# Optimization experiments

Hardware: AMD Instinct MI355X
Metric: run time of the kernel (lower is better)

The kernel has to match this reference:

```python
import jax, jax.numpy as jnp
import numpy as np

B, Q, D, N = 128, 20, 11, 100000  # batch, produced vectors per sample, feature dim, song DB size
EPS = 1e-8  # torch cosine_similarity eps


def setup_inputs() -> dict:
    key = jax.random.key(0)
    ks = jax.random.split(key, 8)
    x = jax.random.normal(ks[0], (B, 5, 11), dtype=jnp.float32)
    W1 = jax.random.normal(ks[1], (55, 128), dtype=jnp.float32) * 0.1
    b1 = jnp.zeros((128,), dtype=jnp.float32)
    W2 = jax.random.normal(ks[2], (128, 64), dtype=jnp.float32) * 0.1
    b2 = jnp.zeros((64,), dtype=jnp.float32)
    W3 = jax.random.normal(ks[3], (64, Q * D), dtype=jnp.float32) * 0.1
    b3 = jnp.zeros((Q * D,), dtype=jnp.float32)
    songs = jax.random.normal(ks[4], (N, D), dtype=jnp.float32)
    return {"x": x, "W1": W1, "b1": b1, "W2": W2, "b2": b2, "W3": W3, "b3": b3, "songs": songs}


def reference(x, W1, b1, W2, b2, W3, b3, songs):
    # Encoder MLP: Flatten -> Linear -> ReLU -> Linear -> ReLU -> Linear
    h = x.reshape(x.shape[0], -1)                 # [B, 55]
    h = jax.nn.relu(h @ W1 + b1)                  # [B, 128]
    h = jax.nn.relu(h @ W2 + b2)                  # [B, 64]
    produced = (h @ W3 + b3).reshape(-1, Q, D)    # [B, 20, 11]

    # Batched cosine-similarity kNN (k=1 / argmax) against the song DB.
    # torch cosine_similarity: a.b / (max(||a||, eps) * max(||b||, eps))
    p_norm = produced / jnp.maximum(jnp.linalg.norm(produced, axis=-1, keepdims=True), EPS)
    s_norm = songs / jnp.maximum(jnp.linalg.norm(songs, axis=-1, keepdims=True), EPS)
    sim = jnp.einsum('bqd,nd->bqn', p_norm, s_norm)  # [B, Q, N]
    best = jnp.argmax(sim, axis=-1)                  # [B, Q]
    return songs[best]                                # [B, Q, D]
```

## Files before the change

kernel.cpp:

```cpp
#include <hip/hip_runtime.h>
#include <math.h>

#define EPS 1e-8f

constexpr int B_ = 128;
constexpr int Q_ = 20;
constexpr int D_ = 11;
constexpr int N_ = 100000;
constexpr int DP_ = 12;
constexpr int NPAIR = B_ * Q_;
constexpr int NCH = 1000;
constexpr int CS = N_ / NCH;
constexpr int NG = CS / 4;
constexpr int STPB = 128;
constexpr int PPT = 4;
constexpr int REP = NPAIR / (PPT * STPB);

__global__ void prep_kernel(const float* __restrict__ x,
                            const float* __restrict__ W1, const float* __restrict__ b1,
                            const float* __restrict__ W2, const float* __restrict__ b2,
                            const float* __restrict__ W3, const float* __restrict__ b3,
                            const float* __restrict__ songs,
                            float* __restrict__ pnorm, float* __restrict__ snorm,
                            int do_snorm)
{
    const int t = threadIdx.x;
    if (blockIdx.x >= B_) {
        if (!do_snorm) return;
        const int i = (blockIdx.x - B_) * blockDim.x + t;
        if (i >= N_) return;
        float v[DP_]; float ss = 0.0f;
#pragma unroll
        for (int d = 0; d < D_; ++d) { v[d] = songs[(size_t)i * D_ + d]; ss += v[d] * v[d]; }
        float nrm = fmaxf(sqrtf(ss), EPS);
#pragma unroll
        for (int d = 0; d < D_; ++d) v[d] /= nrm;
        v[D_] = 0.0f;
        float4* o = reinterpret_cast<float4*>(snorm + (size_t)i * DP_);
        o[0] = make_float4(v[0], v[1], v[2], v[3]);
        o[1] = make_float4(v[4], v[5], v[6], v[7]);
        o[2] = make_float4(v[8], v[9], v[10], v[11]);
        return;
    }
    __shared__ float xr[55];
    __shared__ float h1[128];
    __shared__ float h2[64];
    __shared__ float prod[220];
    const int b = blockIdx.x;
    if (t < 55) xr[t] = x[b * 55 + t];
    __syncthreads();
    if (t < 128) {
        float s = b1[t];
        for (int k = 0; k < 55; ++k) s += xr[k] * W1[k * 128 + t];
        h1[t] = fmaxf(s, 0.0f);
    }
    __syncthreads();
    if (t < 64) {
        float s = b2[t];
        for (int k = 0; k < 128; ++k) s += h1[k] * W2[k * 64 + t];
        h2[t] = fmaxf(s, 0.0f);
    }
    __syncthreads();
    if (t < 220) {
        float s = b3[t];
        for (int k = 0; k < 64; ++k) s += h2[k] * W3[k * 220 + t];
        prod[t] = s;
    }
    __syncthreads();
    if (t < Q_) {
        float ss = 0.0f;
        for (int d = 0; d < D_; ++d) { float v = prod[t * D_ + d]; ss += v * v; }
        float nrm = fmaxf(sqrtf(ss), EPS);
        float* o = pnorm + (b * Q_ + t) * DP_;
        for (int d = 0; d < D_; ++d) o[d] = prod[t * D_ + d] / nrm;
        o[D_] = 0.0f;
    }
}

__device__ __forceinline__ float dot11(const float* __restrict__ q,
                                       const float4 a, const float4 b, const float4 c)
{
    float x = q[0] * a.x;
    x = fmaf(q[1], a.y, x);
    x = fmaf(q[2], a.z, x);
    x = fmaf(q[3], a.w, x);
    x = fmaf(q[4], b.x, x);
    x = fmaf(q[5], b.y, x);
    x = fmaf(q[6], b.z, x);
    x = fmaf(q[7], b.w, x);
    x = fmaf(q[8], c.x, x);
    x = fmaf(q[9], c.y, x);
    x = fmaf(q[10], c.z, x);
    return x;
}

__device__ __forceinline__ unsigned int fkey(float f)
{
    unsigned int b = __float_as_uint(f);
    return (b & 0x80000000u) ? ~b : (b | 0x80000000u);
}

__device__ __forceinline__ unsigned long long pack_vi(float v, int idx)
{
    return ((unsigned long long)fkey(v) << 32) | (unsigned long long)(0xFFFFFFFFu - (unsigned int)idx);
}

__global__ __launch_bounds__(STPB, 4)
void sim7_kernel(const float* __restrict__ pnorm,
                 const float* __restrict__ snorm,
                 unsigned long long* __restrict__ res)
{
    __shared__ __align__(16) float lds[CS * DP_];
    const int bid = blockIdx.x;
    const int u = bid & 7;
    const int k = bid >> 3;
    const int r = k % REP;
    const int m = k / REP;
    const int chunk = u + 8 * m;
    const int t = threadIdx.x;

    const float4* src = reinterpret_cast<const float4*>(snorm) + (size_t)chunk * CS * 3;
    float4* l4 = reinterpret_cast<float4*>(lds);
    for (int i = t; i < CS * 3; i += STPB) l4[i] = src[i];

    const int jb = r * (PPT * STPB) + t;
    float qv[PPT][D_];
#pragma unroll
    for (int p = 0; p < PPT; ++p) {
        const float4* q4 = reinterpret_cast<const float4*>(pnorm + (size_t)(jb + p * STPB) * DP_);
        float4 qa = q4[0], qb = q4[1], qc = q4[2];
        qv[p][0] = qa.x; qv[p][1] = qa.y; qv[p][2]  = qa.z; qv[p][3] = qa.w;
        qv[p][4] = qb.x; qv[p][5] = qb.y; qv[p][6]  = qb.z; qv[p][7] = qb.w;
        qv[p][8] = qc.x; qv[p][9] = qc.y; qv[p][10] = qc.z;
    }
    __syncthreads();

    float bv[PPT]; int gi[PPT];
#pragma unroll
    for (int p = 0; p < PPT; ++p) { bv[p] = -1e30f; gi[p] = 0; }

    const float4* vg = l4;
    for (int g = 0; g < NG; ++g, vg += 12) {
        float4 v0 = vg[0], v1 = vg[1], v2 = vg[2], v3 = vg[3], v4 = vg[4], v5 = vg[5];
        float a0[PPT], a1[PPT];
#pragma unroll
        for (int p = 0; p < PPT; ++p) {
            a0[p] = dot11(qv[p], v0, v1, v2);
            a1[p] = dot11(qv[p], v3, v4, v5);
        }
        float4 w0 = vg[6], w1 = vg[7], w2 = vg[8], w3 = vg[9], w4 = vg[10], w5 = vg[11];
#pragma unroll
        for (int p = 0; p < PPT; ++p) {
            float a2 = dot11(qv[p], w0, w1, w2);
            float a3 = dot11(qv[p], w3, w4, w5);
            float mx = fmaxf(fmaxf(a0[p], a1[p]), fmaxf(a2, a3));
            if (mx > bv[p]) { bv[p] = mx; gi[p] = g; }
        }
    }

#pragma unroll
    for (int p = 0; p < PPT; ++p) {
        const float4* wg = l4 + gi[p] * 12;
        float a0 = dot11(qv[p], wg[0], wg[1],  wg[2]);
        float a1 = dot11(qv[p], wg[3], wg[4],  wg[5]);
        float a2 = dot11(qv[p], wg[6], wg[7],  wg[8]);
        float a3 = dot11(qv[p], wg[9], wg[10], wg[11]);
        int base = chunk * CS + gi[p] * 4;
        int idx = base;
        if (a3 == bv[p]) idx = base + 3;
        if (a2 == bv[p]) idx = base + 2;
        if (a1 == bv[p]) idx = base + 1;
        if (a0 == bv[p]) idx = base;
        atomicMax(&res[jb + p * STPB], pack_vi(bv[p], idx));
    }
}

template<int FNCH>
__global__ void sim6f_kernel(const float* __restrict__ pnorm,
                             const float* __restrict__ songs,
                             unsigned long long* __restrict__ res)
{
    constexpr int FCS = N_ / FNCH;
    const int chunk = blockIdx.x;
    const int j = blockIdx.y * 256 + threadIdx.x;

    float qv[D_];
#pragma unroll
    for (int d = 0; d < D_; ++d) qv[d] = pnorm[j * DP_ + d];

    float bestv = -1e30f;
    int   besti = 0;
    const int base = chunk * FCS;
    for (int i = base; i < base + FCS; ++i) {
        float sv[D_]; float ss = 0.0f;
#pragma unroll
        for (int d = 0; d < D_; ++d) { sv[d] = songs[(size_t)i * D_ + d]; ss += sv[d] * sv[d]; }
        float nrm = fmaxf(sqrtf(ss), EPS);
        float a = qv[0] * (sv[0] / nrm);
#pragma unroll
        for (int d = 1; d < D_; ++d) a = fmaf(qv[d], sv[d] / nrm, a);
        if (a > bestv) { bestv = a; besti = i; }
    }
    atomicMax(&res[j], pack_vi(bestv, besti));
}

__global__ void gather_kernel(const unsigned long long* __restrict__ res,
                              const float* __restrict__ songs, float* __restrict__ out)
{
    const int j = blockIdx.x * blockDim.x + threadIdx.x;
    if (j >= NPAIR) return;
    const unsigned int idx = 0xFFFFFFFFu - (unsigned int)(res[j] & 0xFFFFFFFFull);
#pragma unroll
    for (int d = 0; d < D_; ++d) out[(size_t)j * D_ + d] = songs[(size_t)idx * D_ + d];
}

extern "C" void kernel_launch(void* const* d_in, const int* in_sizes, int n_in,
                              void* d_out, int out_size, void* d_ws, size_t ws_size,
                              hipStream_t stream)
{
    const float* x     = (const float*)d_in[0];
    const float* W1    = (const float*)d_in[1];
    const float* b1    = (const float*)d_in[2];
    const float* W2    = (const float*)d_in[3];
    const float* b2    = (const float*)d_in[4];
    const float* W3    = (const float*)d_in[5];
    const float* b3    = (const float*)d_in[6];
    const float* songs = (const float*)d_in[7];
    float* out = (float*)d_out;

    constexpr size_t PN = (size_t)NPAIR * DP_;
    constexpr size_t SN = (size_t)N_ * DP_;
    float* pnorm = (float*)d_ws;
    constexpr int SNB = (N_ + 255) / 256;

    const size_t need_full = (PN + SN) * sizeof(float) + (size_t)NPAIR * 8 + 64;
    const size_t need_min  = PN * sizeof(float) + (size_t)NPAIR * 8 + 64;

    if (ws_size >= need_full) {
        float* snorm = pnorm + PN;
        unsigned long long* res =
            (unsigned long long*)(((uintptr_t)(snorm + SN) + 7) & ~(uintptr_t)7);
        hipMemsetAsync(res, 0, (size_t)NPAIR * 8, stream);
        prep_kernel<<<B_ + SNB, 256, 0, stream>>>(x, W1, b1, W2, b2, W3, b3, songs,
                                                  pnorm, snorm, 1);
        sim7_kernel<<<NCH * REP, STPB, 0, stream>>>(pnorm, snorm, res);
        gather_kernel<<<(NPAIR + 255) / 256, 256, 0, stream>>>(res, songs, out);
    } else if (ws_size >= need_min) {
        unsigned long long* res =
            (unsigned long long*)(((uintptr_t)(pnorm + PN) + 7) & ~(uintptr_t)7);
        hipMemsetAsync(res, 0, (size_t)NPAIR * 8, stream);
        prep_kernel<<<B_, 256, 0, stream>>>(x, W1, b1, W2, b2, W3, b3, songs,
                                            pnorm, nullptr, 0);
        constexpr int FNCH = 250;
        sim6f_kernel<FNCH><<<dim3(FNCH, NPAIR / 256), 256, 0, stream>>>(pnorm, songs, res);
        gather_kernel<<<(NPAIR + 255) / 256, 256, 0, stream>>>(res, songs, out);
    }
}
```

Measured before the change: 92.78 us.

## Read song vectors directly from global memory with one wavefront per block

Removes the LDS staging of each song chunk and the block barrier, so each 64-thread block (one wavefront) reads the normalized song vectors straight from global memory. The addresses are uniform across the wave, so the compiler can turn them into scalar loads. Pairs per thread rise from 4 to 8 to get more reuse of each loaded song vector. This trades shared-memory traffic and sync for scalar/global loads and higher register pressure under the existing launch bounds.

```diff
diff --git a/kernel.cpp b/kernel.cpp
--- a/kernel.cpp
+++ b/kernel.cpp
@@ -12,8 +12,8 @@
 constexpr int NCH = 1000;
 constexpr int CS = N_ / NCH;
 constexpr int NG = CS / 4;
-constexpr int STPB = 128;
-constexpr int PPT = 4;
+constexpr int STPB = 64;
+constexpr int PPT = 8;
 constexpr int REP = NPAIR / (PPT * STPB);
 
 __global__ void prep_kernel(const float* __restrict__ x,
@@ -77,20 +77,20 @@
     }
 }
 
-__device__ __forceinline__ float dot11(const float* __restrict__ q,
-                                       const float4 a, const float4 b, const float4 c)
-{
-    float x = q[0] * a.x;
-    x = fmaf(q[1], a.y, x);
-    x = fmaf(q[2], a.z, x);
-    x = fmaf(q[3], a.w, x);
-    x = fmaf(q[4], b.x, x);
-    x = fmaf(q[5], b.y, x);
-    x = fmaf(q[6], b.z, x);
-    x = fmaf(q[7], b.w, x);
-    x = fmaf(q[8], c.x, x);
-    x = fmaf(q[9], c.y, x);
-    x = fmaf(q[10], c.z, x);
+__device__ __forceinline__ float dot11s(const float* __restrict__ q,
+                                        const float* __restrict__ s)
+{
+    float x = q[0] * s[0];
+    x = fmaf(q[1],  s[1],  x);
+    x = fmaf(q[2],  s[2],  x);
+    x = fmaf(q[3],  s[3],  x);
+    x = fmaf(q[4],  s[4],  x);
+    x = fmaf(q[5],  s[5],  x);
+    x = fmaf(q[6],  s[6],  x);
+    x = fmaf(q[7],  s[7],  x);
+    x = fmaf(q[8],  s[8],  x);
+    x = fmaf(q[9],  s[9],  x);
+    x = fmaf(q[10], s[10], x);
     return x;
 }
 
@@ -106,24 +106,19 @@
 }
 
 __global__ __launch_bounds__(STPB, 4)
-void sim7_kernel(const float* __restrict__ pnorm,
+void sim8_kernel(const float* __restrict__ pnorm,
                  const float* __restrict__ snorm,
                  unsigned long long* __restrict__ res)
 {
-    __shared__ __align__(16) float lds[CS * DP_];
     const int bid = blockIdx.x;
     const int u = bid & 7;
     const int k = bid >> 3;
     const int r = k % REP;
     const int m = k / REP;
     const int chunk = u + 8 * m;
-    const int t = threadIdx.x;
-
-    const float4* src = reinterpret_cast<const float4*>(snorm) + (size_t)chunk * CS * 3;
-    float4* l4 = reinterpret_cast<float4*>(lds);
-    for (int i = t; i < CS * 3; i += STPB) l4[i] = src[i];
-
-    const int jb = r * (PPT * STPB) + t;
+    const int lane = threadIdx.x;
+
+    const int jb = r * (PPT * STPB) + lane;
     float qv[PPT][D_];
 #pragma unroll
     for (int p = 0; p < PPT; ++p) {
@@ -133,38 +128,33 @@
         qv[p][4] = qb.x; qv[p][5] = qb.y; qv[p][6]  = qb.z; qv[p][7] = qb.w;
         qv[p][8] = qc.x; qv[p][9] = qc.y; qv[p][10] = qc.z;
     }
-    __syncthreads();
 
     float bv[PPT]; int gi[PPT];
 #pragma unroll
     for (int p = 0; p < PPT; ++p) { bv[p] = -1e30f; gi[p] = 0; }
 
-    const float4* vg = l4;
-    for (int g = 0; g < NG; ++g, vg += 12) {
-        float4 v0 = vg[0], v1 = vg[1], v2 = vg[2], v3 = vg[3], v4 = vg[4], v5 = vg[5];
-        float a0[PPT], a1[PPT];
+    const float* cb = snorm + (size_t)chunk * CS * DP_;
+
+    for (int g = 0; g < NG; ++g) {
+        const float* sb = cb + g * (4 * DP_);
 #pragma unroll
         for (int p = 0; p < PPT; ++p) {
-            a0[p] = dot11(qv[p], v0, v1, v2);
-            a1[p] = dot11(qv[p], v3, v4, v5);
-        }
-        float4 w0 = vg[6], w1 = vg[7], w2 = vg[8], w3 = vg[9], w4 = vg[10], w5 = vg[11];
-#pragma unroll
-        for (int p = 0; p < PPT; ++p) {
-            float a2 = dot11(qv[p], w0, w1, w2);
-            float a3 = dot11(qv[p], w3, w4, w5);
-            float mx = fmaxf(fmaxf(a0[p], a1[p]), fmaxf(a2, a3));
+            float a0 = dot11s(qv[p], sb);
+            float a1 = dot11s(qv[p], sb + DP_);
+            float a2 = dot11s(qv[p], sb + 2 * DP_);
+            float a3 = dot11s(qv[p], sb + 3 * DP_);
+            float mx = fmaxf(fmaxf(a0, a1), fmaxf(a2, a3));
             if (mx > bv[p]) { bv[p] = mx; gi[p] = g; }
         }
     }
 
 #pragma unroll
     for (int p = 0; p < PPT; ++p) {
-        const float4* wg = l4 + gi[p] * 12;
-        float a0 = dot11(qv[p], wg[0], wg[1],  wg[2]);
-        float a1 = dot11(qv[p], wg[3], wg[4],  wg[5]);
-        float a2 = dot11(qv[p], wg[6], wg[7],  wg[8]);
-        float a3 = dot11(qv[p], wg[9], wg[10], wg[11]);
+        const float* sb = cb + gi[p] * (4 * DP_);
+        float a0 = dot11s(qv[p], sb);
+        float a1 = dot11s(qv[p], sb + DP_);
+        float a2 = dot11s(qv[p], sb + 2 * DP_);
+        float a3 = dot11s(qv[p], sb + 3 * DP_);
         int base = chunk * CS + gi[p] * 4;
         int idx = base;
         if (a3 == bv[p]) idx = base + 3;
@@ -243,7 +233,7 @@
         hipMemsetAsync(res, 0, (size_t)NPAIR * 8, stream);
         prep_kernel<<<B_ + SNB, 256, 0, stream>>>(x, W1, b1, W2, b2, W3, b3, songs,
                                                   pnorm, snorm, 1);
-        sim7_kernel<<<NCH * REP, STPB, 0, stream>>>(pnorm, snorm, res);
+        sim8_kernel<<<NCH * REP, STPB, 0, stream>>>(pnorm, snorm, res);
         gather_kernel<<<(NPAIR + 255) / 256, 256, 0, stream>>>(res, songs, out);
     } else if (ws_size >= need_min) {
         unsigned long long* res =
```

New measurement: 118.8 us. +28.0%, slower.

## Give each block all query pairs over two song chunks with register prefetch

Applied to the files above, without the earlier changes.

Replaces the sim7 grid (1000 chunks × 5 query groups, 4 queries per thread) with 500 blocks of 256 threads. Each block covers all 2560 query vectors at 10 per thread and walks two song chunks in sequence. The second chunk is loaded into registers while the first chunk is processed, then written to LDS. This raises per-thread register reuse of song vectors, reduces redundant LDS loads of song data, and cuts atomics per song chunk. It costs heavy register pressure (110 query floats per thread), launch bounds of 1, and far fewer resident waves, which can hurt latency hiding.

```diff
diff --git a/kernel.cpp b/kernel.cpp
--- a/kernel.cpp
+++ b/kernel.cpp
@@ -12,9 +12,10 @@
 constexpr int NCH = 1000;
 constexpr int CS = N_ / NCH;
 constexpr int NG = CS / 4;
-constexpr int STPB = 128;
-constexpr int PPT = 4;
-constexpr int REP = NPAIR / (PPT * STPB);
+constexpr int TPB10 = 256;
+constexpr int PPT10 = 10;
+constexpr int CPB = 2;
+constexpr int NBLK = NCH / CPB;
 
 __global__ void prep_kernel(const float* __restrict__ x,
                             const float* __restrict__ W1, const float* __restrict__ b1,
@@ -105,29 +106,56 @@
     return ((unsigned long long)fkey(v) << 32) | (unsigned long long)(0xFFFFFFFFu - (unsigned int)idx);
 }
 
-__global__ __launch_bounds__(STPB, 4)
-void sim7_kernel(const float* __restrict__ pnorm,
-                 const float* __restrict__ snorm,
-                 unsigned long long* __restrict__ res)
-{
-    __shared__ __align__(16) float lds[CS * DP_];
+__device__ __forceinline__ void chunk_pass(const float4* __restrict__ l4,
+                                           const float qv[PPT10][D_],
+                                           float* __restrict__ bv, int* __restrict__ gi,
+                                           int goff)
+{
+    const float4* vg = l4;
+    for (int g = 0; g < NG; ++g, vg += 12) {
+        float4 v0 = vg[0], v1 = vg[1], v2 = vg[2], v3 = vg[3], v4 = vg[4], v5 = vg[5];
+        float a0[PPT10], a1[PPT10];
+#pragma unroll
+        for (int p = 0; p < PPT10; ++p) {
+            a0[p] = dot11(qv[p], v0, v1, v2);
+            a1[p] = dot11(qv[p], v3, v4, v5);
+        }
+        float4 w0 = vg[6], w1 = vg[7], w2 = vg[8], w3 = vg[9], w4 = vg[10], w5 = vg[11];
+#pragma unroll
+        for (int p = 0; p < PPT10; ++p) {
+            float a2 = dot11(qv[p], w0, w1, w2);
+            float a3 = dot11(qv[p], w3, w4, w5);
+            float mx = fmaxf(fmaxf(a0[p], a1[p]), fmaxf(a2, a3));
+            if (mx > bv[p]) { bv[p] = mx; gi[p] = goff + g; }
+        }
+    }
+}
+
+__global__ __launch_bounds__(TPB10, 1)
+void sim10_kernel(const float* __restrict__ pnorm,
+                  const float* __restrict__ snorm,
+                  unsigned long long* __restrict__ res)
+{
+    __shared__ __align__(16) float lds[CPB][CS * DP_];
     const int bid = blockIdx.x;
-    const int u = bid & 7;
-    const int k = bid >> 3;
-    const int r = k % REP;
-    const int m = k / REP;
-    const int chunk = u + 8 * m;
     const int t = threadIdx.x;
-
-    const float4* src = reinterpret_cast<const float4*>(snorm) + (size_t)chunk * CS * 3;
-    float4* l4 = reinterpret_cast<float4*>(lds);
-    for (int i = t; i < CS * 3; i += STPB) l4[i] = src[i];
-
-    const int jb = r * (PPT * STPB) + t;
-    float qv[PPT][D_];
-#pragma unroll
-    for (int p = 0; p < PPT; ++p) {
-        const float4* q4 = reinterpret_cast<const float4*>(pnorm + (size_t)(jb + p * STPB) * DP_);
+    const int c0 = bid * CPB;
+
+    const float4* s40 = reinterpret_cast<const float4*>(snorm) + (size_t)c0 * CS * 3;
+    const float4* s41 = s40 + CS * 3;
+    float4* b0 = reinterpret_cast<float4*>(lds[0]);
+    float4* b1 = reinterpret_cast<float4*>(lds[1]);
+
+    b0[t] = s40[t];
+    if (t < CS * 3 - TPB10) b0[t + TPB10] = s40[t + TPB10];
+    float4 r0 = s41[t];
+    float4 r1 = make_float4(0.f, 0.f, 0.f, 0.f);
+    if (t < CS * 3 - TPB10) r1 = s41[t + TPB10];
+
+    float qv[PPT10][D_];
+#pragma unroll
+    for (int p = 0; p < PPT10; ++p) {
+        const float4* q4 = reinterpret_cast<const float4*>(pnorm + (size_t)(t + p * TPB10) * DP_);
         float4 qa = q4[0], qb = q4[1], qc = q4[2];
         qv[p][0] = qa.x; qv[p][1] = qa.y; qv[p][2]  = qa.z; qv[p][3] = qa.w;
         qv[p][4] = qb.x; qv[p][5] = qb.y; qv[p][6]  = qb.z; qv[p][7] = qb.w;
@@ -135,43 +163,35 @@
     }
     __syncthreads();
 
-    float bv[PPT]; int gi[PPT];
-#pragma unroll
-    for (int p = 0; p < PPT; ++p) { bv[p] = -1e30f; gi[p] = 0; }
-
-    const float4* vg = l4;
-    for (int g = 0; g < NG; ++g, vg += 12) {
-        float4 v0 = vg[0], v1 = vg[1], v2 = vg[2], v3 = vg[3], v4 = vg[4], v5 = vg[5];
-        float a0[PPT], a1[PPT];
-#pragma unroll
-        for (int p = 0; p < PPT; ++p) {
-            a0[p] = dot11(qv[p], v0, v1, v2);
-            a1[p] = dot11(qv[p], v3, v4, v5);
-        }
-        float4 w0 = vg[6], w1 = vg[7], w2 = vg[8], w3 = vg[9], w4 = vg[10], w5 = vg[11];
-#pragma unroll
-        for (int p = 0; p < PPT; ++p) {
-            float a2 = dot11(qv[p], w0, w1, w2);
-            float a3 = dot11(qv[p], w3, w4, w5);
-            float mx = fmaxf(fmaxf(a0[p], a1[p]), fmaxf(a2, a3));
-            if (mx > bv[p]) { bv[p] = mx; gi[p] = g; }
-        }
-    }
-
-#pragma unroll
-    for (int p = 0; p < PPT; ++p) {
-        const float4* wg = l4 + gi[p] * 12;
+    float bv[PPT10]; int gi[PPT10];
+#pragma unroll
+    for (int p = 0; p < PPT10; ++p) { bv[p] = -1e30f; gi[p] = 0; }
+
+    chunk_pass(b0, qv, bv, gi, 0);
+
+    b1[t] = r0;
+    if (t < CS * 3 - TPB10) b1[t + TPB10] = r1;
+    __syncthreads();
+
+    chunk_pass(b1, qv, bv, gi, NG);
+
+#pragma unroll
+    for (int p = 0; p < PPT10; ++p) {
+        const int gsel = gi[p];
+        const int cs = (gsel >= NG) ? 1 : 0;
+        const int gg = gsel - cs * NG;
+        const float4* wg = reinterpret_cast<const float4*>(lds[cs]) + gg * 12;
         float a0 = dot11(qv[p], wg[0], wg[1],  wg[2]);
         float a1 = dot11(qv[p], wg[3], wg[4],  wg[5]);
         float a2 = dot11(qv[p], wg[6], wg[7],  wg[8]);
         float a3 = dot11(qv[p], wg[9], wg[10], wg[11]);
-        int base = chunk * CS + gi[p] * 4;
+        const int base = (c0 + cs) * CS + gg * 4;
         int idx = base;
         if (a3 == bv[p]) idx = base + 3;
         if (a2 == bv[p]) idx = base + 2;
         if (a1 == bv[p]) idx = base + 1;
         if (a0 == bv[p]) idx = base;
-        atomicMax(&res[jb + p * STPB], pack_vi(bv[p], idx));
+        atomicMax(&res[t + p * TPB10], pack_vi(bv[p], idx));
     }
 }
 
@@ -243,7 +263,7 @@
         hipMemsetAsync(res, 0, (size_t)NPAIR * 8, stream);
         prep_kernel<<<B_ + SNB, 256, 0, stream>>>(x, W1, b1, W2, b2, W3, b3, songs,
                                                   pnorm, snorm, 1);
-        sim7_kernel<<<NCH * REP, STPB, 0, stream>>>(pnorm, snorm, res);
+        sim10_kernel<<<NBLK, TPB10, 0, stream>>>(pnorm, snorm, res);
         gather_kernel<<<(NPAIR + 255) / 256, 256, 0, stream>>>(res, songs, out);
     } else if (ws_size >= need_min) {
         unsigned long long* res =
```

New measurement: 97.64 us. +5.2%, slower.
